# Optimization experiments

Hardware: AMD Instinct MI355X
Metric: run time of the kernel (lower is better)

Reference implementation:

```python
import jax, jax.numpy as jnp
import numpy as np

B, C, T, H = 32, 256, 512, 8
EPS = 1e-5
NEG_INF = jnp.float32(-1e9)


def setup_inputs() -> dict:
    key = jax.random.key(0)
    ks = jax.random.split(key, 10)
    inp = {
        "seq": jax.random.normal(ks[0], (B, C, T), dtype=jnp.float32),
        "mask": jax.random.randint(ks[1], (B, T), 0, 2, dtype=jnp.int32),
        "Wq": jax.random.normal(ks[2], (C, C), dtype=jnp.float32) * 0.05,
        "bq": jnp.zeros((C,), dtype=jnp.float32),
        "Wk": jax.random.normal(ks[3], (C, C), dtype=jnp.float32) * 0.05,
        "bk": jnp.zeros((C,), dtype=jnp.float32),
        "Wv": jax.random.normal(ks[4], (C, C), dtype=jnp.float32) * 0.05,
        "bv": jnp.zeros((C,), dtype=jnp.float32),
        "gamma": jnp.ones((C,), dtype=jnp.float32),
        "beta": jnp.zeros((C,), dtype=jnp.float32),
    }
    return inp


def reference(seq, mask, Wq, bq, Wk, bk, Wv, bv, gamma, beta):
    d = C // H  # per-head dim
    s = jnp.transpose(seq, (0, 2, 1))  # [B, T, C]
    # ReLU'd projections (torch Linear: x @ W.T + b)
    Q = jax.nn.relu(s @ Wq.T + bq)
    K = jax.nn.relu(s @ Wk.T + bk)
    V = jax.nn.relu(s @ Wv.T + bv)
    # head split: channel block h -> head h (torch cat(split, dim=0) order = h*B+b)
    Qh = Q.reshape(B, T, H, d).transpose(2, 0, 1, 3)  # [H, B, T, d]
    Kh = K.reshape(B, T, H, d).transpose(2, 0, 1, 3)
    Vh = V.reshape(B, T, H, d).transpose(2, 0, 1, 3)
    scores = jnp.einsum('hbtd,hbsd->hbts', Qh, Kh) / jnp.sqrt(jnp.float32(d))
    # additive key mask before softmax
    key_mask = (mask == 0)[None, :, None, :]  # [1, B, 1, T]
    scores = jnp.where(key_mask, NEG_INF, scores)
    # multiplicative query mask after softmax
    qmask = mask.astype(jnp.float32)[None, :, :, None]  # [1, B, T, 1]
    att = jax.nn.softmax(scores, axis=-1) * qmask
    # dropout with keep_prob=1.0 is identity
    o = jnp.einsum('hbts,hbsd->hbtd', att, Vh)  # [H, B, T, d]
    x = o.transpose(1, 2, 0, 3).reshape(B, T, C)  # heads concatenated on channels
    x = jnp.transpose(x, (0, 2, 1))  # [B, C, T]
    # BatchNorm(pre_mask=True, post_mask=is_mask=True), training-mode batch stats
    m = (mask == 1)[:, None, :]  # [B, 1, T]
    x = jnp.where(m, x, jnp.float32(0.0))
    mean = jnp.mean(x, axis=(0, 2))
    var = jnp.mean((x - mean[None, :, None]) ** 2, axis=(0, 2))  # biased var (torch BN)
    xn = (x - mean[None, :, None]) * jax.lax.rsqrt(var + EPS)[None, :, None]
    x = gamma[None, :, None] * xn + beta[None, :, None]
    x = jnp.where(m, x, jnp.float32(0.0))
    return x
```

## Files before the change

kernel.cpp:

```cpp
#include <hip/hip_runtime.h>
#include <math.h>

#define NB 32
#define NC 256
#define NT 512
#define NH 8
#define ND 32
#define SCALE 0.17677669529663687f

typedef __attribute__((ext_vector_type(8))) __bf16 bf16x8;
typedef __attribute__((ext_vector_type(4))) __bf16 bf16x4;
typedef __attribute__((ext_vector_type(4))) float  f32x4;

static __device__ __forceinline__ f32x4 mfma16x16x32(bf16x8 a, bf16x8 b, f32x4 c) {
    return __builtin_amdgcn_mfma_f32_16x16x32_bf16(a, b, c, 0, 0, 0);
}

__global__ __launch_bounds__(256) void qkv_mfma(
    const float* __restrict__ seq,
    const float* __restrict__ Wq, const float* __restrict__ bq,
    const float* __restrict__ Wk, const float* __restrict__ bk,
    const float* __restrict__ Wv, const float* __restrict__ bv,
    __bf16* __restrict__ Qh, __bf16* __restrict__ Kh, __bf16* __restrict__ Vh,
    float* __restrict__ stats)
{
    __shared__ __bf16 As[64][264];
    __shared__ __bf16 Ws[3][64][40];

    const int tid = threadIdx.x;
    const int t0  = blockIdx.x * 64;
    const int co0 = blockIdx.y * 64;
    const int bb  = blockIdx.z;

    if (blockIdx.x == 0 && blockIdx.y == 0 && bb == 0 && tid < 128)
        ((float4*)stats)[tid] = make_float4(0.f, 0.f, 0.f, 0.f);

    {
        const int cl = tid & 15;
        const int t4 = (tid >> 4) * 4;
        for (int it = 0; it < 16; ++it) {
            const int c = it*16 + cl;
            const float4 v = *(const float4*)&seq[((size_t)(bb*NC + c))*NT + t0 + t4];
            As[t4+0][c] = (__bf16)v.x;
            As[t4+1][c] = (__bf16)v.y;
            As[t4+2][c] = (__bf16)v.z;
            As[t4+3][c] = (__bf16)v.w;
        }
    }

    const float* Wp[3] = {Wq, Wk, Wv};

    f32x4 acc[3][4];
    #pragma unroll
    for (int p = 0; p < 3; ++p)
        #pragma unroll
        for (int n = 0; n < 4; ++n) acc[p][n] = (f32x4)0.f;

    const int l   = tid & 63;
    const int w   = tid >> 6;
    const int lr  = l & 15;
    const int lk8 = (l >> 4) * 8;

    int wp_[6], wco[6], wc4[6];
    #pragma unroll
    for (int i = 0; i < 6; ++i) {
        const int lin = i*256 + tid;
        wp_[i] = lin >> 9;
        const int r = lin & 511;
        wco[i] = r >> 3;
        wc4[i] = (r & 7) * 4;
    }

    float4 wreg[6];
    #pragma unroll
    for (int i = 0; i < 6; ++i)
        wreg[i] = *(const float4*)&Wp[wp_[i]][(size_t)(co0 + wco[i])*NC + wc4[i]];

    for (int kc = 0; kc < 8; ++kc) {
        __syncthreads();
        #pragma unroll
        for (int i = 0; i < 6; ++i) {
            bf16x4 wb;
            wb[0] = (__bf16)wreg[i].x; wb[1] = (__bf16)wreg[i].y;
            wb[2] = (__bf16)wreg[i].z; wb[3] = (__bf16)wreg[i].w;
            *(bf16x4*)&Ws[wp_[i]][wco[i]][wc4[i]] = wb;
        }
        __syncthreads();

        if (kc < 7) {
            #pragma unroll
            for (int i = 0; i < 6; ++i)
                wreg[i] = *(const float4*)&Wp[wp_[i]][(size_t)(co0 + wco[i])*NC + (kc+1)*32 + wc4[i]];
        }

        const bf16x8 a = *(const bf16x8*)&As[w*16 + lr][kc*32 + lk8];
        #pragma unroll
        for (int p = 0; p < 3; ++p)
            #pragma unroll
            for (int n = 0; n < 4; ++n) {
                const bf16x8 bfr = *(const bf16x8*)&Ws[p][n*16 + lr][lk8];
                acc[p][n] = mfma16x16x32(a, bfr, acc[p][n]);
            }
    }

    const float* bias[3] = {bq, bk, bv};
    __bf16* outp[3] = {Qh, Kh, Vh};
    #pragma unroll
    for (int p = 0; p < 3; ++p) {
        #pragma unroll
        for (int n = 0; n < 4; ++n) {
            const int c  = co0 + n*16 + lr;
            const int hh = c >> 5, jj = c & 31;
            const float bv_ = bias[p][c];
            const float sc  = (p == 0) ? SCALE : 1.f;
            __bf16* op = outp[p] + ((size_t)(bb*NH + hh)*NT)*ND + jj;
            #pragma unroll
            for (int r = 0; r < 4; ++r) {
                const int t = t0 + w*16 + (l>>4)*4 + r;
                op[(size_t)t*ND] = (__bf16)(fmaxf(acc[p][n][r] + bv_, 0.f) * sc);
            }
        }
    }
}

__global__ __launch_bounds__(256) void attn_mfma(
    const __bf16* __restrict__ Qh, const __bf16* __restrict__ Kh,
    const __bf16* __restrict__ Vh, const int* __restrict__ mask,
    float* __restrict__ xout, float* __restrict__ stats)
{
    __shared__ __bf16 Qs[128][40];
    __shared__ __bf16 Ks[64][40];
    __shared__ __bf16 VTs[32][72];
    __shared__ float  Sb[128][68];
    __shared__ __bf16 PA[128][72];
    __shared__ int    smask[64];
    __shared__ float  rowf[128];
    __shared__ float  rowl[128];
    __shared__ float  bnsum[32][4];
    __shared__ float  bnsum2[32][4];

    const int tid = threadIdx.x;
    const int t0  = blockIdx.x * 128;
    const int h   = blockIdx.y;
    const int bb  = blockIdx.z;
    const int bh  = bb*NH + h;
    const __bf16* Qp = Qh + (size_t)bh*NT*ND;
    const __bf16* Kp = Kh + (size_t)bh*NT*ND;
    const __bf16* Vp = Vh + (size_t)bh*NT*ND;

    #pragma unroll
    for (int it = 0; it < 2; ++it) {
        const int idx = it*256 + tid;
        const int t = idx >> 2, c8 = (idx & 3) * 8;
        *(uint4*)&Qs[t][c8] = *(const uint4*)&Qp[(size_t)(t0 + t)*ND + c8];
    }

    const int l   = tid & 63;
    const int w   = tid >> 6;
    const int lr  = l & 15;
    const int lk8 = (l >> 4) * 8;
    const int sm_row = tid >> 1, sm_li = tid & 1;

    f32x4 accO[2][2];
    #pragma unroll
    for (int tt = 0; tt < 2; ++tt)
        #pragma unroll
        for (int jt = 0; jt < 2; ++jt) accO[tt][jt] = (f32x4)0.f;
    float m_run = -1e30f, l_run = 0.f;

    const int kv_s = tid >> 2, kv_c8 = (tid & 3) * 8;

    for (int s0 = 0; s0 < NT; s0 += 64) {
        const uint4 kreg = *(const uint4*)&Kp[(size_t)(s0 + kv_s)*ND + kv_c8];
        ushort4 vreg[2];
        #pragma unroll
        for (int it = 0; it < 2; ++it) {
            const int lin = it*256 + tid;
            const int s = lin >> 3, j4 = (lin & 7) * 4;
            vreg[it] = *(const ushort4*)&Vp[(size_t)(s0 + s)*ND + j4];
        }
        const int mreg = (tid < 64) ? mask[bb*NT + s0 + tid] : 0;

        __syncthreads();
        *(uint4*)&Ks[kv_s][kv_c8] = kreg;
        #pragma unroll
        for (int it = 0; it < 2; ++it) {
            const int lin = it*256 + tid;
            const int s = lin >> 3, j4 = (lin & 7) * 4;
            const __bf16* vb = (const __bf16*)&vreg[it];
            VTs[j4+0][s] = vb[0]; VTs[j4+1][s] = vb[1];
            VTs[j4+2][s] = vb[2]; VTs[j4+3][s] = vb[3];
        }
        if (tid < 64) smask[tid] = mreg;
        __syncthreads();

        {
            bf16x8 aq[2];
            aq[0] = *(const bf16x8*)&Qs[w*32      + lr][lk8];
            aq[1] = *(const bf16x8*)&Qs[w*32 + 16 + lr][lk8];
            #pragma unroll
            for (int n = 0; n < 4; ++n) {
                const bf16x8 bk_ = *(const bf16x8*)&Ks[n*16 + lr][lk8];
                const int km = smask[n*16 + lr];
                const int col = n*16 + lr;
                #pragma unroll
                for (int tt = 0; tt < 2; ++tt) {
                    const f32x4 s_ = mfma16x16x32(aq[tt], bk_, (f32x4)0.f);
                    const int row = w*32 + tt*16 + (l>>4)*4;
                    #pragma unroll
                    for (int r = 0; r < 4; ++r)
                        Sb[row + r][col] = km ? s_[r] : -1e9f;
                }
            }
        }
        __syncthreads();

        {
            float vals[32];
            float mx = -1e30f;
            #pragma unroll
            for (int k4 = 0; k4 < 8; ++k4) {
                const float4 v = *(const float4*)&Sb[sm_row][sm_li*32 + k4*4];
                vals[k4*4+0] = v.x; vals[k4*4+1] = v.y;
                vals[k4*4+2] = v.z; vals[k4*4+3] = v.w;
                mx = fmaxf(mx, fmaxf(fmaxf(v.x, v.y), fmaxf(v.z, v.w)));
            }
            mx = fmaxf(mx, __shfl_xor(mx, 1));
            const float m_new = fmaxf(m_run, mx);
            const float f = __expf(m_run - m_new);
            float ssum = 0.f;
            #pragma unroll
            for (int k = 0; k < 32; ++k) {
                vals[k] = __expf(vals[k] - m_new);
                ssum += vals[k];
            }
            #pragma unroll
            for (int k4 = 0; k4 < 8; ++k4) {
                bf16x4 pb;
                pb[0] = (__bf16)vals[k4*4+0]; pb[1] = (__bf16)vals[k4*4+1];
                pb[2] = (__bf16)vals[k4*4+2]; pb[3] = (__bf16)vals[k4*4+3];
                *(bf16x4*)&PA[sm_row][sm_li*32 + k4*4] = pb;
            }
            ssum += __shfl_xor(ssum, 1);
            l_run = l_run*f + ssum;
            m_run = m_new;
            if (sm_li == 0) rowf[sm_row] = f;
        }
        __syncthreads();

        {
            float fr[2][4];
            #pragma unroll
            for (int tt = 0; tt < 2; ++tt)
                #pragma unroll
                for (int r = 0; r < 4; ++r)
                    fr[tt][r] = rowf[w*32 + tt*16 + (l>>4)*4 + r];
            #pragma unroll
            for (int tt = 0; tt < 2; ++tt)
                #pragma unroll
                for (int jt = 0; jt < 2; ++jt)
                    #pragma unroll
                    for (int r = 0; r < 4; ++r)
                        accO[tt][jt][r] *= fr[tt][r];

            #pragma unroll
            for (int kh = 0; kh < 2; ++kh) {
                bf16x8 pa[2], vb[2];
                pa[0] = *(const bf16x8*)&PA[w*32      + lr][kh*32 + lk8];
                pa[1] = *(const bf16x8*)&PA[w*32 + 16 + lr][kh*32 + lk8];
                vb[0] = *(const bf16x8*)&VTs[     lr][kh*32 + lk8];
                vb[1] = *(const bf16x8*)&VTs[16 + lr][kh*32 + lk8];
                #pragma unroll
                for (int tt = 0; tt < 2; ++tt)
                    #pragma unroll
                    for (int jt = 0; jt < 2; ++jt)
                        accO[tt][jt] = mfma16x16x32(pa[tt], vb[jt], accO[tt][jt]);
            }
        }
    }

    if (sm_li == 0)
        rowl[sm_row] = mask[bb*NT + t0 + sm_row] ? (1.f / l_run) : 0.f;
    __syncthreads();

    float psum[2] = {0.f, 0.f}, psq[2] = {0.f, 0.f};
    #pragma unroll
    for (int tt = 0; tt < 2; ++tt) {
        const int rbase = w*32 + tt*16 + (l>>4)*4;
        float rl[4];
        #pragma unroll
        for (int r = 0; r < 4; ++r) rl[r] = rowl[rbase + r];
        #pragma unroll
        for (int jt = 0; jt < 2; ++jt) {
            const int c = h*ND + jt*16 + lr;
            float4 o;
            o.x = accO[tt][jt][0]*rl[0];
            o.y = accO[tt][jt][1]*rl[1];
            o.z = accO[tt][jt][2]*rl[2];
            o.w = accO[tt][jt][3]*rl[3];
            *(float4*)&xout[((size_t)(bb*NC + c))*NT + t0 + rbase] = o;
            psum[jt] += o.x + o.y + o.z + o.w;
            psq[jt]  += o.x*o.x + o.y*o.y + o.z*o.z + o.w*o.w;
        }
    }
    #pragma unroll
    for (int jt = 0; jt < 2; ++jt) {
        psum[jt] += __shfl_xor(psum[jt], 16);
        psum[jt] += __shfl_xor(psum[jt], 32);
        psq[jt]  += __shfl_xor(psq[jt], 16);
        psq[jt]  += __shfl_xor(psq[jt], 32);
    }
    if (l < 16) {
        bnsum [l     ][w] = psum[0];  bnsum2[l     ][w] = psq[0];
        bnsum [l + 16][w] = psum[1];  bnsum2[l + 16][w] = psq[1];
    }
    __syncthreads();
    if (tid < 32) {
        const float s  = bnsum [tid][0] + bnsum [tid][1] + bnsum [tid][2] + bnsum [tid][3];
        const float s2 = bnsum2[tid][0] + bnsum2[tid][1] + bnsum2[tid][2] + bnsum2[tid][3];
        atomicAdd(&stats[h*ND + tid], s);
        atomicAdd(&stats[NC + h*ND + tid], s2);
    }
}

__global__ __launch_bounds__(256) void bn_apply_kernel(
    float* __restrict__ x, const float* __restrict__ stats,
    const float* __restrict__ gamma, const float* __restrict__ beta,
    const int* __restrict__ mask)
{
    const int idx = blockIdx.x*256 + threadIdx.x;
    const int t4 = idx & 127;
    const int c  = (idx >> 7) & 255;
    const int bb = idx >> 15;
    float4 v = ((const float4*)x)[idx];
    const int4 mk = *(const int4*)&mask[bb*NT + t4*4];
    const float mean = stats[c] * (1.f/16384.f);
    const float var  = fmaxf(stats[NC + c]*(1.f/16384.f) - mean*mean, 0.f);
    const float rstd = rsqrtf(var + 1e-5f);
    const float g = gamma[c], be = beta[c];
    v.x = mk.x ? fmaf((v.x - mean)*rstd, g, be) : 0.f;
    v.y = mk.y ? fmaf((v.y - mean)*rstd, g, be) : 0.f;
    v.z = mk.z ? fmaf((v.z - mean)*rstd, g, be) : 0.f;
    v.w = mk.w ? fmaf((v.w - mean)*rstd, g, be) : 0.f;
    ((float4*)x)[idx] = v;
}

extern "C" void kernel_launch(void* const* d_in, const int* in_sizes, int n_in,
                              void* d_out, int out_size, void* d_ws, size_t ws_size,
                              hipStream_t stream)
{
    const float* seq   = (const float*)d_in[0];
    const int*   mask  = (const int*)  d_in[1];
    const float* Wq    = (const float*)d_in[2];
    const float* bq    = (const float*)d_in[3];
    const float* Wk    = (const float*)d_in[4];
    const float* bk    = (const float*)d_in[5];
    const float* Wv    = (const float*)d_in[6];
    const float* bv    = (const float*)d_in[7];
    const float* gamma = (const float*)d_in[8];
    const float* beta  = (const float*)d_in[9];
    float* out = (float*)d_out;

    const size_t perMat = (size_t)NB*NH*NT*ND;
    __bf16* Qh = (__bf16*)d_ws;
    __bf16* Kh = Qh + perMat;
    __bf16* Vh = Kh + perMat;
    float* stats = (float*)(Vh + perMat);

    qkv_mfma<<<dim3(NT/64, NC/64, NB), 256, 0, stream>>>(
        seq, Wq, bq, Wk, bk, Wv, bv, Qh, Kh, Vh, stats);
    attn_mfma<<<dim3(NT/128, NH, NB), 256, 0, stream>>>(
        Qh, Kh, Vh, mask, out, stats);
    bn_apply_kernel<<<dim3((NB*NC*NT/4)/256), 256, 0, stream>>>(
        out, stats, gamma, beta, mask);
}
```

Baseline: 157.3 us.

## Keep attention scores in registers via transposed MFMA and per-lane softmax

Reworks the attention kernel to compute S^T = K·Q^T so each lane holds a full column of scores for one query row. Softmax then runs in registers with cross-lane shuffles instead of going through a shared-memory score buffer, removing two block barriers per KV tile. The key mask becomes a wave ballot bitmask, and Q is loaded straight into registers. The Q projection is prescaled by log2(e) so exp2f replaces __expf. The price is more shuffle traffic and strided scalar output stores in the epilogue in place of float4 stores.

```diff
diff --git a/kernel.cpp b/kernel.cpp
--- a/kernel.cpp
+++ b/kernel.cpp
@@ -7,6 +7,9 @@
 #define NH 8
 #define ND 32
 #define SCALE 0.17677669529663687f
+#define LOG2E 1.4426950408889634f
+#define QSCALE (SCALE * LOG2E)
+#define MASKVAL (-1.4426950408889634e9f)
 
 typedef __attribute__((ext_vector_type(8))) __bf16 bf16x8;
 typedef __attribute__((ext_vector_type(4))) __bf16 bf16x4;
@@ -112,7 +115,7 @@
             const int c  = co0 + n*16 + lr;
             const int hh = c >> 5, jj = c & 31;
             const float bv_ = bias[p][c];
-            const float sc  = (p == 0) ? SCALE : 1.f;
+            const float sc  = (p == 0) ? QSCALE : 1.f;
             __bf16* op = outp[p] + ((size_t)(bb*NH + hh)*NT)*ND + jj;
             #pragma unroll
             for (int r = 0; r < 4; ++r) {
@@ -128,14 +131,9 @@
     const __bf16* __restrict__ Vh, const int* __restrict__ mask,
     float* __restrict__ xout, float* __restrict__ stats)
 {
-    __shared__ __bf16 Qs[128][40];
     __shared__ __bf16 Ks[64][40];
     __shared__ __bf16 VTs[32][72];
-    __shared__ float  Sb[128][68];
     __shared__ __bf16 PA[128][72];
-    __shared__ int    smask[64];
-    __shared__ float  rowf[128];
-    __shared__ float  rowl[128];
     __shared__ float  bnsum[32][4];
     __shared__ float  bnsum2[32][4];
 
@@ -148,25 +146,24 @@
     const __bf16* Kp = Kh + (size_t)bh*NT*ND;
     const __bf16* Vp = Vh + (size_t)bh*NT*ND;
 
-    #pragma unroll
-    for (int it = 0; it < 2; ++it) {
-        const int idx = it*256 + tid;
-        const int t = idx >> 2, c8 = (idx & 3) * 8;
-        *(uint4*)&Qs[t][c8] = *(const uint4*)&Qp[(size_t)(t0 + t)*ND + c8];
-    }
-
     const int l   = tid & 63;
     const int w   = tid >> 6;
     const int lr  = l & 15;
-    const int lk8 = (l >> 4) * 8;
-    const int sm_row = tid >> 1, sm_li = tid & 1;
+    const int g   = l >> 4;
+    const int lk8 = g * 8;
+
+    bf16x8 qb[2];
+    #pragma unroll
+    for (int ct = 0; ct < 2; ++ct)
+        qb[ct] = *(const bf16x8*)&Qp[(size_t)(t0 + w*32 + ct*16 + lr)*ND + lk8];
 
     f32x4 accO[2][2];
     #pragma unroll
-    for (int tt = 0; tt < 2; ++tt)
-        #pragma unroll
-        for (int jt = 0; jt < 2; ++jt) accO[tt][jt] = (f32x4)0.f;
-    float m_run = -1e30f, l_run = 0.f;
+    for (int jt = 0; jt < 2; ++jt)
+        #pragma unroll
+        for (int ct = 0; ct < 2; ++ct) accO[jt][ct] = (f32x4)0.f;
+    float m_run[2] = {-1e30f, -1e30f};
+    float l_run[2] = {0.f, 0.f};
 
     const int kv_s = tid >> 2, kv_c8 = (tid & 3) * 8;
 
@@ -179,7 +176,7 @@
             const int s = lin >> 3, j4 = (lin & 7) * 4;
             vreg[it] = *(const ushort4*)&Vp[(size_t)(s0 + s)*ND + j4];
         }
-        const int mreg = (tid < 64) ? mask[bb*NT + s0 + tid] : 0;
+        const unsigned long long mw = __ballot(mask[bb*NT + s0 + l] != 0);
 
         __syncthreads();
         *(uint4*)&Ks[kv_s][kv_c8] = kreg;
@@ -191,128 +188,118 @@
             VTs[j4+0][s] = vb[0]; VTs[j4+1][s] = vb[1];
             VTs[j4+2][s] = vb[2]; VTs[j4+3][s] = vb[3];
         }
-        if (tid < 64) smask[tid] = mreg;
         __syncthreads();
 
-        {
-            bf16x8 aq[2];
-            aq[0] = *(const bf16x8*)&Qs[w*32      + lr][lk8];
-            aq[1] = *(const bf16x8*)&Qs[w*32 + 16 + lr][lk8];
-            #pragma unroll
-            for (int n = 0; n < 4; ++n) {
-                const bf16x8 bk_ = *(const bf16x8*)&Ks[n*16 + lr][lk8];
-                const int km = smask[n*16 + lr];
-                const int col = n*16 + lr;
+        bf16x8 kA[4];
+        #pragma unroll
+        for (int st = 0; st < 4; ++st)
+            kA[st] = *(const bf16x8*)&Ks[st*16 + lr][lk8];
+
+        #pragma unroll
+        for (int ct = 0; ct < 2; ++ct) {
+            f32x4 sst[4];
+            #pragma unroll
+            for (int st = 0; st < 4; ++st)
+                sst[st] = mfma16x16x32(kA[st], qb[ct], (f32x4)0.f);
+
+            float v[16];
+            float mx = -1e30f;
+            #pragma unroll
+            for (int st = 0; st < 4; ++st)
                 #pragma unroll
-                for (int tt = 0; tt < 2; ++tt) {
-                    const f32x4 s_ = mfma16x16x32(aq[tt], bk_, (f32x4)0.f);
-                    const int row = w*32 + tt*16 + (l>>4)*4;
-                    #pragma unroll
-                    for (int r = 0; r < 4; ++r)
-                        Sb[row + r][col] = km ? s_[r] : -1e9f;
+                for (int r = 0; r < 4; ++r) {
+                    const int s = st*16 + g*4 + r;
+                    const float val = ((mw >> s) & 1ull) ? sst[st][r] : MASKVAL;
+                    v[st*4+r] = val;
+                    mx = fmaxf(mx, val);
                 }
-            }
-        }
-        __syncthreads();
-
-        {
-            float vals[32];
-            float mx = -1e30f;
-            #pragma unroll
-            for (int k4 = 0; k4 < 8; ++k4) {
-                const float4 v = *(const float4*)&Sb[sm_row][sm_li*32 + k4*4];
-                vals[k4*4+0] = v.x; vals[k4*4+1] = v.y;
-                vals[k4*4+2] = v.z; vals[k4*4+3] = v.w;
-                mx = fmaxf(mx, fmaxf(fmaxf(v.x, v.y), fmaxf(v.z, v.w)));
-            }
-            mx = fmaxf(mx, __shfl_xor(mx, 1));
-            const float m_new = fmaxf(m_run, mx);
-            const float f = __expf(m_run - m_new);
+            mx = fmaxf(mx, __shfl_xor(mx, 16));
+            mx = fmaxf(mx, __shfl_xor(mx, 32));
+            const float m_new = fmaxf(m_run[ct], mx);
+            const float f = exp2f(m_run[ct] - m_new);
+
+            const int trow = w*32 + ct*16 + lr;
             float ssum = 0.f;
             #pragma unroll
-            for (int k = 0; k < 32; ++k) {
-                vals[k] = __expf(vals[k] - m_new);
-                ssum += vals[k];
-            }
-            #pragma unroll
-            for (int k4 = 0; k4 < 8; ++k4) {
-                bf16x4 pb;
-                pb[0] = (__bf16)vals[k4*4+0]; pb[1] = (__bf16)vals[k4*4+1];
-                pb[2] = (__bf16)vals[k4*4+2]; pb[3] = (__bf16)vals[k4*4+3];
-                *(bf16x4*)&PA[sm_row][sm_li*32 + k4*4] = pb;
-            }
-            ssum += __shfl_xor(ssum, 1);
-            l_run = l_run*f + ssum;
-            m_run = m_new;
-            if (sm_li == 0) rowf[sm_row] = f;
-        }
-        __syncthreads();
-
-        {
-            float fr[2][4];
-            #pragma unroll
-            for (int tt = 0; tt < 2; ++tt)
+            for (int st = 0; st < 4; ++st) {
+                bf16x4 pb4;
+                #pragma unroll
+                for (int r = 0; r < 4; ++r) {
+                    const float p = exp2f(v[st*4+r] - m_new);
+                    ssum += p;
+                    pb4[r] = (__bf16)p;
+                }
+                *(bf16x4*)&PA[trow][st*16 + g*4] = pb4;
+            }
+            ssum += __shfl_xor(ssum, 16);
+            ssum += __shfl_xor(ssum, 32);
+            l_run[ct] = l_run[ct]*f + ssum;
+            m_run[ct] = m_new;
+
+            #pragma unroll
+            for (int jt = 0; jt < 2; ++jt)
                 #pragma unroll
                 for (int r = 0; r < 4; ++r)
-                    fr[tt][r] = rowf[w*32 + tt*16 + (l>>4)*4 + r];
-            #pragma unroll
-            for (int tt = 0; tt < 2; ++tt)
+                    accO[jt][ct][r] *= f;
+        }
+
+        #pragma unroll
+        for (int kh = 0; kh < 2; ++kh) {
+            bf16x8 va[2], pb[2];
+            #pragma unroll
+            for (int jt = 0; jt < 2; ++jt)
+                va[jt] = *(const bf16x8*)&VTs[jt*16 + lr][kh*32 + lk8];
+            #pragma unroll
+            for (int ct = 0; ct < 2; ++ct)
+                pb[ct] = *(const bf16x8*)&PA[w*32 + ct*16 + lr][kh*32 + lk8];
+            #pragma unroll
+            for (int jt = 0; jt < 2; ++jt)
                 #pragma unroll
-                for (int jt = 0; jt < 2; ++jt)
-                    #pragma unroll
-                    for (int r = 0; r < 4; ++r)
-                        accO[tt][jt][r] *= fr[tt][r];
-
-            #pragma unroll
-            for (int kh = 0; kh < 2; ++kh) {
-                bf16x8 pa[2], vb[2];
-                pa[0] = *(const bf16x8*)&PA[w*32      + lr][kh*32 + lk8];
-                pa[1] = *(const bf16x8*)&PA[w*32 + 16 + lr][kh*32 + lk8];
-                vb[0] = *(const bf16x8*)&VTs[     lr][kh*32 + lk8];
-                vb[1] = *(const bf16x8*)&VTs[16 + lr][kh*32 + lk8];
-                #pragma unroll
-                for (int tt = 0; tt < 2; ++tt)
-                    #pragma unroll
-                    for (int jt = 0; jt < 2; ++jt)
-                        accO[tt][jt] = mfma16x16x32(pa[tt], vb[jt], accO[tt][jt]);
-            }
-        }
-    }
-
-    if (sm_li == 0)
-        rowl[sm_row] = mask[bb*NT + t0 + sm_row] ? (1.f / l_run) : 0.f;
-    __syncthreads();
-
-    float psum[2] = {0.f, 0.f}, psq[2] = {0.f, 0.f};
-    #pragma unroll
-    for (int tt = 0; tt < 2; ++tt) {
-        const int rbase = w*32 + tt*16 + (l>>4)*4;
-        float rl[4];
-        #pragma unroll
-        for (int r = 0; r < 4; ++r) rl[r] = rowl[rbase + r];
+                for (int ct = 0; ct < 2; ++ct)
+                    accO[jt][ct] = mfma16x16x32(va[jt], pb[ct], accO[jt][ct]);
+        }
+    }
+
+    float psum[2][4], psq[2][4];
+    #pragma unroll
+    for (int jt = 0; jt < 2; ++jt)
+        #pragma unroll
+        for (int r = 0; r < 4; ++r) { psum[jt][r] = 0.f; psq[jt][r] = 0.f; }
+
+    #pragma unroll
+    for (int ct = 0; ct < 2; ++ct) {
+        const int t = t0 + w*32 + ct*16 + lr;
+        const float rl = mask[bb*NT + t] ? (1.f / l_run[ct]) : 0.f;
         #pragma unroll
         for (int jt = 0; jt < 2; ++jt) {
-            const int c = h*ND + jt*16 + lr;
-            float4 o;
-            o.x = accO[tt][jt][0]*rl[0];
-            o.y = accO[tt][jt][1]*rl[1];
-            o.z = accO[tt][jt][2]*rl[2];
-            o.w = accO[tt][jt][3]*rl[3];
-            *(float4*)&xout[((size_t)(bb*NC + c))*NT + t0 + rbase] = o;
-            psum[jt] += o.x + o.y + o.z + o.w;
-            psq[jt]  += o.x*o.x + o.y*o.y + o.z*o.z + o.w*o.w;
-        }
-    }
-    #pragma unroll
-    for (int jt = 0; jt < 2; ++jt) {
-        psum[jt] += __shfl_xor(psum[jt], 16);
-        psum[jt] += __shfl_xor(psum[jt], 32);
-        psq[jt]  += __shfl_xor(psq[jt], 16);
-        psq[jt]  += __shfl_xor(psq[jt], 32);
-    }
-    if (l < 16) {
-        bnsum [l     ][w] = psum[0];  bnsum2[l     ][w] = psq[0];
-        bnsum [l + 16][w] = psum[1];  bnsum2[l + 16][w] = psq[1];
+            #pragma unroll
+            for (int r = 0; r < 4; ++r) {
+                const int c = h*ND + jt*16 + g*4 + r;
+                const float o = accO[jt][ct][r] * rl;
+                xout[((size_t)(bb*NC + c))*NT + t] = o;
+                psum[jt][r] += o;
+                psq[jt][r]  += o*o;
+            }
+        }
+    }
+    #pragma unroll
+    for (int jt = 0; jt < 2; ++jt)
+        #pragma unroll
+        for (int r = 0; r < 4; ++r) {
+            #pragma unroll
+            for (int off = 1; off < 16; off <<= 1) {
+                psum[jt][r] += __shfl_xor(psum[jt][r], off);
+                psq[jt][r]  += __shfl_xor(psq[jt][r],  off);
+            }
+        }
+    if (lr == 0) {
+        #pragma unroll
+        for (int jt = 0; jt < 2; ++jt)
+            #pragma unroll
+            for (int r = 0; r < 4; ++r) {
+                bnsum [jt*16 + g*4 + r][w] = psum[jt][r];
+                bnsum2[jt*16 + g*4 + r][w] = psq[jt][r];
+            }
     }
     __syncthreads();
     if (tid < 32) {
```

New measurement: 156.2 us. Within noise of the previous version (-0.7%).
